# Kernel tuning notes

Hardware: AMD Instinct MI355X
Metric: run time of the kernel (lower is better)

Reference implementation:

```python
import jax, jax.numpy as jnp
import numpy as np

N_NODES = 262144
N_GRAPHS = 1024
FEAT = 256


def setup_inputs() -> dict:
    key = jax.random.key(0)
    ks = jax.random.split(key, 12)
    F = FEAT
    inp = {
        "node_feats": jax.random.normal(ks[0], (N_NODES, F), jnp.float32),
        "g_feats": jax.random.normal(ks[1], (N_GRAPHS, F), jnp.float32),
        "segment_ids": jnp.sort(jax.random.randint(ks[2], (N_NODES,), 0, N_GRAPHS, jnp.int32)),
        "num_graphs": N_GRAPHS,
        # compute_logits: Linear(2F, 1)
        "logit_w": jax.random.normal(ks[3], (1, 2 * F), jnp.float32) / np.sqrt(2 * F),
        "logit_b": jnp.zeros((1,), jnp.float32),
        # project_nodes: Linear(F, F) (dropout is identity at eval)
        "proj_w": jax.random.normal(ks[4], (F, F), jnp.float32) / np.sqrt(F),
        "proj_b": jnp.zeros((F,), jnp.float32),
        # GRUCell(F, F): weight_ih [3F, F], weight_hh [3F, F]
        "w_ih": jax.random.normal(ks[5], (3 * F, F), jnp.float32) / np.sqrt(F),
        "w_hh": jax.random.normal(ks[6], (3 * F, F), jnp.float32) / np.sqrt(F),
        "b_ih": jnp.zeros((3 * F,), jnp.float32),
        "b_hh": jnp.zeros((3 * F,), jnp.float32),
    }
    return inp


def _gru_cell(x, h, w_ih, w_hh, b_ih, b_hh):
    gi = x @ w_ih.T + b_ih          # [B, 3F]
    gh = h @ w_hh.T + b_hh          # [B, 3F]
    i_r, i_z, i_n = jnp.split(gi, 3, axis=-1)
    h_r, h_z, h_n = jnp.split(gh, 3, axis=-1)
    r = jax.nn.sigmoid(i_r + h_r)
    z = jax.nn.sigmoid(i_z + h_z)
    n = jnp.tanh(i_n + r * h_n)
    return (1.0 - z) * n + z * h


def reference(node_feats, g_feats, segment_ids, num_graphs,
              logit_w, logit_b, proj_w, proj_b, w_ih, w_hh, b_ih, b_hh):
    # broadcast_nodes(g, relu(g_feats)) -> gather per-graph feats to nodes
    bcast = jax.nn.relu(g_feats)[segment_ids]                    # [N, F]
    cat = jnp.concatenate([bcast, node_feats], axis=-1)          # [N, 2F]
    z = jax.nn.leaky_relu(cat @ logit_w.T + logit_b, 0.01)       # [N, 1]
    # segment softmax over nodes of each graph (dgl.softmax_nodes)
    zf = z[:, 0]
    m = jax.ops.segment_max(zf, segment_ids, num_segments=num_graphs)
    e = jnp.exp(zf - m[segment_ids])
    s = jax.ops.segment_sum(e, segment_ids, num_segments=num_graphs)
    a = (e / s[segment_ids])[:, None]                            # [N, 1]
    # project_nodes (dropout = identity at eval)
    hv = node_feats @ proj_w.T + proj_b                          # [N, F]
    # attention-weighted segment sum (dgl.sum_nodes with weight 'a')
    g_repr = jax.ops.segment_sum(a * hv, segment_ids, num_segments=num_graphs)  # [B, F]
    return _gru_cell(jax.nn.elu(g_repr), g_feats, w_ih, w_hh, b_ih, b_hh)
```

## Files before the change

### kernel.cpp

```cpp
#include <hip/hip_runtime.h>
#include <hip/hip_bf16.h>
#include <cstdint>

#define N_NODES  262144
#define N_GRAPHS 1024
#define FEAT     256

using short8 = __attribute__((ext_vector_type(8))) short;
using f32x4  = __attribute__((ext_vector_type(4))) float;

#define MFMA_BF16 __builtin_amdgcn_mfma_f32_16x16x32_bf16

__device__ __forceinline__ unsigned short f2bf(float f){
    unsigned u = __float_as_uint(f);
    u = u + 0x7FFFu + ((u >> 16) & 1u);
    return (unsigned short)(u >> 16);
}
__device__ __forceinline__ float sigmoidf_(float x){ return 1.0f/(1.0f+__expf(-x)); }

__global__ __launch_bounds__(256) void glogit_kernel(
        const float* __restrict__ gf, const float* __restrict__ lw,
        const float* __restrict__ lb, float* __restrict__ glog){
    int wid  = (blockIdx.x*blockDim.x + threadIdx.x) >> 6;
    int lane = threadIdx.x & 63;
    if (wid >= N_GRAPHS) return;
    float4 g = ((const float4*)gf)[wid*64 + lane];
    float4 w = ((const float4*)lw)[lane];
    float p = fmaxf(g.x,0.f)*w.x + fmaxf(g.y,0.f)*w.y +
              fmaxf(g.z,0.f)*w.z + fmaxf(g.w,0.f)*w.w;
    #pragma unroll
    for (int m=1;m<64;m<<=1) p += __shfl_xor(p, m, 64);
    if (lane==0) glog[wid] = p + lb[0];
}

__global__ __launch_bounds__(256) void convert_kernel(
        const float* __restrict__ gf,  const float* __restrict__ pw,
        const float* __restrict__ wih, const float* __restrict__ whh,
        unsigned short* __restrict__ h_bf,  unsigned short* __restrict__ pw_bf,
        unsigned short* __restrict__ wih_bf, unsigned short* __restrict__ whh_bf){
    int i = blockIdx.x*blockDim.x + threadIdx.x;
    const float* src; unsigned short* dst; int base;
    if      (i <  65536){ src=gf;  dst=h_bf;   base=i;        }
    else if (i <  81920){ src=pw;  dst=pw_bf;  base=i-65536;  }
    else if (i < 131072){ src=wih; dst=wih_bf; base=i-81920;  }
    else                { src=whh; dst=whh_bf; base=i-131072; }
    float4 v = ((const float4*)src)[base];
    ushort4 o; o.x=f2bf(v.x); o.y=f2bf(v.y); o.z=f2bf(v.z); o.w=f2bf(v.w);
    ((ushort4*)dst)[base] = o;
}

__global__ __launch_bounds__(256) void pass1_kernel(
        const float* __restrict__ nf, const int* __restrict__ seg,
        const float* __restrict__ glog, const float* __restrict__ lw1,
        float* __restrict__ num, float* __restrict__ den){
    const int NPW = 32;
    int wid  = (blockIdx.x*blockDim.x + threadIdx.x) >> 6;
    int lane = threadIdx.x & 63;
    int n0   = wid * NPW;
    float4 w4 = ((const float4*)lw1)[lane];
    const float4* nf4 = (const float4*)nf;

    float a0=0.f,a1=0.f,a2=0.f,a3=0.f,dacc=0.f;
    int   cur = seg[n0];
    float gl  = glog[cur];
    float4 x  = nf4[(size_t)n0*64 + lane];
    int    s  = cur;

    for (int i=0;i<NPW;i++){
        float4 xc = x; int sc = s;
        if (i+1 < NPW){
            x = nf4[(size_t)(n0+i+1)*64 + lane];
            s = seg[n0+i+1];
        }
        if (sc != cur){
            atomicAdd(&num[cur*FEAT + lane*4+0], a0);
            atomicAdd(&num[cur*FEAT + lane*4+1], a1);
            atomicAdd(&num[cur*FEAT + lane*4+2], a2);
            atomicAdd(&num[cur*FEAT + lane*4+3], a3);
            if (lane==0) atomicAdd(&den[cur], dacc);
            a0=a1=a2=a3=0.f; dacc=0.f; cur=sc; gl=glog[sc];
        }
        float p = xc.x*w4.x + xc.y*w4.y + xc.z*w4.z + xc.w*w4.w;
        #pragma unroll
        for (int m=1;m<64;m<<=1) p += __shfl_xor(p, m, 64);
        float q  = gl + p;
        float zf = q > 0.f ? q : 0.01f*q;
        float e  = __expf(zf);
        a0 += e*xc.x; a1 += e*xc.y; a2 += e*xc.z; a3 += e*xc.w;
        if (lane==0) dacc += e;
    }
    atomicAdd(&num[cur*FEAT + lane*4+0], a0);
    atomicAdd(&num[cur*FEAT + lane*4+1], a1);
    atomicAdd(&num[cur*FEAT + lane*4+2], a2);
    atomicAdd(&num[cur*FEAT + lane*4+3], a3);
    if (lane==0) atomicAdd(&den[cur], dacc);
}

__global__ __launch_bounds__(256) void gemm1_kernel(
        const float* __restrict__ num, const float* __restrict__ den,
        const unsigned short* __restrict__ pw_bf, const float* __restrict__ pb,
        unsigned short* __restrict__ x_bf){
    int wid  = (blockIdx.x*blockDim.x + threadIdx.x) >> 6;
    int lane = threadIdx.x & 63;
    int rtile = (wid >> 4) * 16;
    int ctile = (wid & 15) * 16;
    int arow = rtile + (lane & 15);
    int brow = ctile + (lane & 15);
    int kgrp = (lane >> 4) * 8;
    float dv  = den[arow];
    float inv = dv > 0.f ? 1.0f/dv : 0.f;
    f32x4 acc = {0.f,0.f,0.f,0.f};
    #pragma unroll
    for (int kk=0; kk<FEAT; kk+=32){
        int kb = kk + kgrp;
        float4 u0 = *(const float4*)(num + arow*FEAT + kb);
        float4 u1 = *(const float4*)(num + arow*FEAT + kb + 4);
        short8 af;
        af[0]=(short)f2bf(u0.x*inv); af[1]=(short)f2bf(u0.y*inv);
        af[2]=(short)f2bf(u0.z*inv); af[3]=(short)f2bf(u0.w*inv);
        af[4]=(short)f2bf(u1.x*inv); af[5]=(short)f2bf(u1.y*inv);
        af[6]=(short)f2bf(u1.z*inv); af[7]=(short)f2bf(u1.w*inv);
        short8 bfr = *(const short8*)(pw_bf + brow*FEAT + kb);
        acc = MFMA_BF16(af, bfr, acc, 0, 0, 0);
    }
    #pragma unroll
    for (int r=0;r<4;r++){
        int row = rtile + (lane>>4)*4 + r;
        int col = ctile + (lane & 15);
        float g  = acc[r] + pb[col];
        float xv = g > 0.f ? g : (__expf(g) - 1.0f);
        x_bf[row*FEAT + col] = f2bf(xv);
    }
}

__global__ __launch_bounds__(256) void gemm2_kernel(
        const unsigned short* __restrict__ x_bf, const unsigned short* __restrict__ h_bf,
        const unsigned short* __restrict__ wih_bf, const unsigned short* __restrict__ whh_bf,
        const float* __restrict__ bih, const float* __restrict__ bhh,
        const float* __restrict__ gf, float* __restrict__ out){
    int wid  = (blockIdx.x*blockDim.x + threadIdx.x) >> 6;
    int lane = threadIdx.x & 63;
    int rtile = (wid >> 4) * 16;
    int ctile = (wid & 15) * 16;
    int arow = rtile + (lane & 15);
    int wrow = ctile + (lane & 15);
    int kgrp = (lane >> 4) * 8;
    f32x4 ir={0,0,0,0}, iz={0,0,0,0}, inn={0,0,0,0};
    f32x4 hr={0,0,0,0}, hz={0,0,0,0}, hnn={0,0,0,0};
    #pragma unroll
    for (int kk=0; kk<FEAT; kk+=32){
        int kb = kk + kgrp;
        short8 ax  = *(const short8*)(x_bf  + arow*FEAT + kb);
        short8 ah  = *(const short8*)(h_bf  + arow*FEAT + kb);
        short8 bir = *(const short8*)(wih_bf + (wrow      )*FEAT + kb);
        short8 biz = *(const short8*)(wih_bf + (wrow + 256)*FEAT + kb);
        short8 bin = *(const short8*)(wih_bf + (wrow + 512)*FEAT + kb);
        short8 bhr = *(const short8*)(whh_bf + (wrow      )*FEAT + kb);
        short8 bhz = *(const short8*)(whh_bf + (wrow + 256)*FEAT + kb);
        short8 bhn = *(const short8*)(whh_bf + (wrow + 512)*FEAT + kb);
        ir  = MFMA_BF16(ax, bir, ir , 0,0,0);
        iz  = MFMA_BF16(ax, biz, iz , 0,0,0);
        inn = MFMA_BF16(ax, bin, inn, 0,0,0);
        hr  = MFMA_BF16(ah, bhr, hr , 0,0,0);
        hz  = MFMA_BF16(ah, bhz, hz , 0,0,0);
        hnn = MFMA_BF16(ah, bhn, hnn, 0,0,0);
    }
    #pragma unroll
    for (int r=0;r<4;r++){
        int row = rtile + (lane>>4)*4 + r;
        int col = ctile + (lane & 15);
        float vir = ir [r] + bih[col      ];
        float viz = iz [r] + bih[col + 256];
        float vin = inn[r] + bih[col + 512];
        float vhr = hr [r] + bhh[col      ];
        float vhz = hz [r] + bhh[col + 256];
        float vhn = hnn[r] + bhh[col + 512];
        float rg = sigmoidf_(vir + vhr);
        float zg = sigmoidf_(viz + vhz);
        float ng = tanhf(vin + rg*vhn);
        float h  = gf[row*FEAT + col];
        out[row*FEAT + col] = (1.f - zg)*ng + zg*h;
    }
}

extern "C" void kernel_launch(void* const* d_in, const int* in_sizes, int n_in,
                              void* d_out, int out_size, void* d_ws, size_t ws_size,
                              hipStream_t stream){
    const float* nf  = (const float*)d_in[0];
    const float* gf  = (const float*)d_in[1];
    const int*   seg = (const int*)  d_in[2];
    const float* lw  = (const float*)d_in[4];
    const float* lb  = (const float*)d_in[5];
    const float* pw  = (const float*)d_in[6];
    const float* pb  = (const float*)d_in[7];
    const float* wih = (const float*)d_in[8];
    const float* whh = (const float*)d_in[9];
    const float* bih = (const float*)d_in[10];
    const float* bhh = (const float*)d_in[11];
    float* out = (float*)d_out;

    float* num  = (float*)d_ws;
    float* den  = num + N_GRAPHS*FEAT;
    float* glog = den + N_GRAPHS;
    unsigned short* h_bf   = (unsigned short*)(glog + N_GRAPHS);
    unsigned short* pw_bf  = h_bf   + N_GRAPHS*FEAT;
    unsigned short* wih_bf = pw_bf  + FEAT*FEAT;
    unsigned short* whh_bf = wih_bf + 3*FEAT*FEAT;
    unsigned short* x_bf   = whh_bf + 3*FEAT*FEAT;

    hipMemsetAsync(d_ws, 0, (size_t)(N_GRAPHS*FEAT + N_GRAPHS)*sizeof(float), stream);
    glogit_kernel <<<N_GRAPHS/4, 256, 0, stream>>>(gf, lw, lb, glog);
    convert_kernel<<<704,        256, 0, stream>>>(gf, pw, wih, whh, h_bf, pw_bf, wih_bf, whh_bf);
    pass1_kernel  <<<2048,       256, 0, stream>>>(nf, seg, glog, lw + FEAT, num, den);
    gemm1_kernel  <<<256,        256, 0, stream>>>(num, den, pw_bf, pb, x_bf);
    gemm2_kernel  <<<256,        256, 0, stream>>>(x_bf, h_bf, wih_bf, whh_bf, bih, bhh, gf, out);
}
```

Baseline: 410.1 us.

## Merge prep kernels, fuse both GEMMs via LDS, use nontemporal node loads

The memset, the graph-logit kernel and the weight-conversion kernel become one prep launch that zeroes the accumulators with regular stores. The projection GEMM plus ELU and the GRU GEMM are fused into one kernel: each block computes a 16-row slab of the projected features into shared memory and then runs the GRU gates on it, so the x_bf round trip through global memory goes away. The node-feature stream in pass1 uses nontemporal loads to reduce cache pollution. The trade-off is fewer launches and less traffic against only 64 blocks for the fused GEMM, which lowers parallelism in that stage.

```diff
diff --git a/kernel.cpp b/kernel.cpp
--- a/kernel.cpp
+++ b/kernel.cpp
@@ -18,35 +18,39 @@
 }
 __device__ __forceinline__ float sigmoidf_(float x){ return 1.0f/(1.0f+__expf(-x)); }
 
-__global__ __launch_bounds__(256) void glogit_kernel(
-        const float* __restrict__ gf, const float* __restrict__ lw,
-        const float* __restrict__ lb, float* __restrict__ glog){
-    int wid  = (blockIdx.x*blockDim.x + threadIdx.x) >> 6;
-    int lane = threadIdx.x & 63;
-    if (wid >= N_GRAPHS) return;
-    float4 g = ((const float4*)gf)[wid*64 + lane];
-    float4 w = ((const float4*)lw)[lane];
-    float p = fmaxf(g.x,0.f)*w.x + fmaxf(g.y,0.f)*w.y +
-              fmaxf(g.z,0.f)*w.z + fmaxf(g.w,0.f)*w.w;
-    #pragma unroll
-    for (int m=1;m<64;m<<=1) p += __shfl_xor(p, m, 64);
-    if (lane==0) glog[wid] = p + lb[0];
-}
-
-__global__ __launch_bounds__(256) void convert_kernel(
+__global__ __launch_bounds__(256) void prep_kernel(
         const float* __restrict__ gf,  const float* __restrict__ pw,
         const float* __restrict__ wih, const float* __restrict__ whh,
+        const float* __restrict__ lw,  const float* __restrict__ lb,
         unsigned short* __restrict__ h_bf,  unsigned short* __restrict__ pw_bf,
-        unsigned short* __restrict__ wih_bf, unsigned short* __restrict__ whh_bf){
-    int i = blockIdx.x*blockDim.x + threadIdx.x;
-    const float* src; unsigned short* dst; int base;
-    if      (i <  65536){ src=gf;  dst=h_bf;   base=i;        }
-    else if (i <  81920){ src=pw;  dst=pw_bf;  base=i-65536;  }
-    else if (i < 131072){ src=wih; dst=wih_bf; base=i-81920;  }
-    else                { src=whh; dst=whh_bf; base=i-131072; }
-    float4 v = ((const float4*)src)[base];
-    ushort4 o; o.x=f2bf(v.x); o.y=f2bf(v.y); o.z=f2bf(v.z); o.w=f2bf(v.w);
-    ((ushort4*)dst)[base] = o;
+        unsigned short* __restrict__ wih_bf, unsigned short* __restrict__ whh_bf,
+        float* __restrict__ num, float* __restrict__ glog){
+    int b = blockIdx.x;
+    if (b < 704){
+        int i = b*256 + threadIdx.x;
+        const float* src; unsigned short* dst; int base;
+        if      (i <  65536){ src=gf;  dst=h_bf;   base=i;        }
+        else if (i <  81920){ src=pw;  dst=pw_bf;  base=i-65536;  }
+        else if (i < 131072){ src=wih; dst=wih_bf; base=i-81920;  }
+        else                { src=whh; dst=whh_bf; base=i-131072; }
+        float4 v = ((const float4*)src)[base];
+        ushort4 o; o.x=f2bf(v.x); o.y=f2bf(v.y); o.z=f2bf(v.z); o.w=f2bf(v.w);
+        ((ushort4*)dst)[base] = o;
+    } else if (b < 961){
+        int i = (b-704)*256 + threadIdx.x;
+        float4 z = {0.f,0.f,0.f,0.f};
+        ((float4*)num)[i] = z;
+    } else {
+        int wid  = (b-961)*4 + (threadIdx.x >> 6);
+        int lane = threadIdx.x & 63;
+        float4 g = ((const float4*)gf)[wid*64 + lane];
+        float4 w = ((const float4*)lw)[lane];
+        float p = fmaxf(g.x,0.f)*w.x + fmaxf(g.y,0.f)*w.y +
+                  fmaxf(g.z,0.f)*w.z + fmaxf(g.w,0.f)*w.w;
+        #pragma unroll
+        for (int m=1;m<64;m<<=1) p += __shfl_xor(p, m, 64);
+        if (lane==0) glog[wid] = p + lb[0];
+    }
 }
 
 __global__ __launch_bounds__(256) void pass1_kernel(
@@ -57,19 +61,19 @@
     int wid  = (blockIdx.x*blockDim.x + threadIdx.x) >> 6;
     int lane = threadIdx.x & 63;
     int n0   = wid * NPW;
-    float4 w4 = ((const float4*)lw1)[lane];
-    const float4* nf4 = (const float4*)nf;
+    f32x4 w4 = ((const f32x4*)lw1)[lane];
+    const f32x4* nf4 = (const f32x4*)nf;
 
     float a0=0.f,a1=0.f,a2=0.f,a3=0.f,dacc=0.f;
     int   cur = seg[n0];
     float gl  = glog[cur];
-    float4 x  = nf4[(size_t)n0*64 + lane];
+    f32x4 x   = __builtin_nontemporal_load(nf4 + (size_t)n0*64 + lane);
     int    s  = cur;
 
     for (int i=0;i<NPW;i++){
-        float4 xc = x; int sc = s;
+        f32x4 xc = x; int sc = s;
         if (i+1 < NPW){
-            x = nf4[(size_t)(n0+i+1)*64 + lane];
+            x = __builtin_nontemporal_load(nf4 + (size_t)(n0+i+1)*64 + lane);
             s = seg[n0+i+1];
         }
         if (sc != cur){
@@ -80,13 +84,13 @@
             if (lane==0) atomicAdd(&den[cur], dacc);
             a0=a1=a2=a3=0.f; dacc=0.f; cur=sc; gl=glog[sc];
         }
-        float p = xc.x*w4.x + xc.y*w4.y + xc.z*w4.z + xc.w*w4.w;
+        float p = xc[0]*w4[0] + xc[1]*w4[1] + xc[2]*w4[2] + xc[3]*w4[3];
         #pragma unroll
         for (int m=1;m<64;m<<=1) p += __shfl_xor(p, m, 64);
         float q  = gl + p;
         float zf = q > 0.f ? q : 0.01f*q;
         float e  = __expf(zf);
-        a0 += e*xc.x; a1 += e*xc.y; a2 += e*xc.z; a3 += e*xc.w;
+        a0 += e*xc[0]; a1 += e*xc[1]; a2 += e*xc[2]; a3 += e*xc[3];
         if (lane==0) dacc += e;
     }
     atomicAdd(&num[cur*FEAT + lane*4+0], a0);
@@ -96,90 +100,100 @@
     if (lane==0) atomicAdd(&den[cur], dacc);
 }
 
-__global__ __launch_bounds__(256) void gemm1_kernel(
+__global__ __launch_bounds__(256) void gemm_fused_kernel(
         const float* __restrict__ num, const float* __restrict__ den,
         const unsigned short* __restrict__ pw_bf, const float* __restrict__ pb,
-        unsigned short* __restrict__ x_bf){
-    int wid  = (blockIdx.x*blockDim.x + threadIdx.x) >> 6;
-    int lane = threadIdx.x & 63;
-    int rtile = (wid >> 4) * 16;
-    int ctile = (wid & 15) * 16;
-    int arow = rtile + (lane & 15);
-    int brow = ctile + (lane & 15);
-    int kgrp = (lane >> 4) * 8;
-    float dv  = den[arow];
-    float inv = dv > 0.f ? 1.0f/dv : 0.f;
-    f32x4 acc = {0.f,0.f,0.f,0.f};
-    #pragma unroll
-    for (int kk=0; kk<FEAT; kk+=32){
-        int kb = kk + kgrp;
-        float4 u0 = *(const float4*)(num + arow*FEAT + kb);
-        float4 u1 = *(const float4*)(num + arow*FEAT + kb + 4);
-        short8 af;
-        af[0]=(short)f2bf(u0.x*inv); af[1]=(short)f2bf(u0.y*inv);
-        af[2]=(short)f2bf(u0.z*inv); af[3]=(short)f2bf(u0.w*inv);
-        af[4]=(short)f2bf(u1.x*inv); af[5]=(short)f2bf(u1.y*inv);
-        af[6]=(short)f2bf(u1.z*inv); af[7]=(short)f2bf(u1.w*inv);
-        short8 bfr = *(const short8*)(pw_bf + brow*FEAT + kb);
-        acc = MFMA_BF16(af, bfr, acc, 0, 0, 0);
-    }
-    #pragma unroll
-    for (int r=0;r<4;r++){
-        int row = rtile + (lane>>4)*4 + r;
-        int col = ctile + (lane & 15);
-        float g  = acc[r] + pb[col];
-        float xv = g > 0.f ? g : (__expf(g) - 1.0f);
-        x_bf[row*FEAT + col] = f2bf(xv);
-    }
-}
-
-__global__ __launch_bounds__(256) void gemm2_kernel(
-        const unsigned short* __restrict__ x_bf, const unsigned short* __restrict__ h_bf,
+        const unsigned short* __restrict__ h_bf,
         const unsigned short* __restrict__ wih_bf, const unsigned short* __restrict__ whh_bf,
         const float* __restrict__ bih, const float* __restrict__ bhh,
         const float* __restrict__ gf, float* __restrict__ out){
-    int wid  = (blockIdx.x*blockDim.x + threadIdx.x) >> 6;
+    __shared__ unsigned short x_s[16][264];
+    int r0   = blockIdx.x * 16;
+    int wave = threadIdx.x >> 6;
     int lane = threadIdx.x & 63;
-    int rtile = (wid >> 4) * 16;
-    int ctile = (wid & 15) * 16;
-    int arow = rtile + (lane & 15);
-    int wrow = ctile + (lane & 15);
+    int rq   = lane & 15;
     int kgrp = (lane >> 4) * 8;
-    f32x4 ir={0,0,0,0}, iz={0,0,0,0}, inn={0,0,0,0};
-    f32x4 hr={0,0,0,0}, hz={0,0,0,0}, hnn={0,0,0,0};
-    #pragma unroll
-    for (int kk=0; kk<FEAT; kk+=32){
-        int kb = kk + kgrp;
-        short8 ax  = *(const short8*)(x_bf  + arow*FEAT + kb);
-        short8 ah  = *(const short8*)(h_bf  + arow*FEAT + kb);
-        short8 bir = *(const short8*)(wih_bf + (wrow      )*FEAT + kb);
-        short8 biz = *(const short8*)(wih_bf + (wrow + 256)*FEAT + kb);
-        short8 bin = *(const short8*)(wih_bf + (wrow + 512)*FEAT + kb);
-        short8 bhr = *(const short8*)(whh_bf + (wrow      )*FEAT + kb);
-        short8 bhz = *(const short8*)(whh_bf + (wrow + 256)*FEAT + kb);
-        short8 bhn = *(const short8*)(whh_bf + (wrow + 512)*FEAT + kb);
-        ir  = MFMA_BF16(ax, bir, ir , 0,0,0);
-        iz  = MFMA_BF16(ax, biz, iz , 0,0,0);
-        inn = MFMA_BF16(ax, bin, inn, 0,0,0);
-        hr  = MFMA_BF16(ah, bhr, hr , 0,0,0);
-        hz  = MFMA_BF16(ah, bhz, hz , 0,0,0);
-        hnn = MFMA_BF16(ah, bhn, hnn, 0,0,0);
-    }
-    #pragma unroll
-    for (int r=0;r<4;r++){
-        int row = rtile + (lane>>4)*4 + r;
-        int col = ctile + (lane & 15);
-        float vir = ir [r] + bih[col      ];
-        float viz = iz [r] + bih[col + 256];
-        float vin = inn[r] + bih[col + 512];
-        float vhr = hr [r] + bhh[col      ];
-        float vhz = hz [r] + bhh[col + 256];
-        float vhn = hnn[r] + bhh[col + 512];
-        float rg = sigmoidf_(vir + vhr);
-        float zg = sigmoidf_(viz + vhz);
-        float ng = tanhf(vin + rg*vhn);
-        float h  = gf[row*FEAT + col];
-        out[row*FEAT + col] = (1.f - zg)*ng + zg*h;
+    int arow = r0 + rq;
+
+    float dv  = den[arow];
+    float inv = dv > 0.f ? 1.0f/dv : 0.f;
+    short8 af[8];
+    #pragma unroll
+    for (int t=0;t<8;t++){
+        int kb = t*32 + kgrp;
+        float4 u0 = *(const float4*)(num + arow*FEAT + kb);
+        float4 u1 = *(const float4*)(num + arow*FEAT + kb + 4);
+        af[t][0]=(short)f2bf(u0.x*inv); af[t][1]=(short)f2bf(u0.y*inv);
+        af[t][2]=(short)f2bf(u0.z*inv); af[t][3]=(short)f2bf(u0.w*inv);
+        af[t][4]=(short)f2bf(u1.x*inv); af[t][5]=(short)f2bf(u1.y*inv);
+        af[t][6]=(short)f2bf(u1.z*inv); af[t][7]=(short)f2bf(u1.w*inv);
+    }
+    #pragma unroll
+    for (int j=0;j<4;j++){
+        int ct = wave*4 + j;
+        int brow = ct*16 + rq;
+        f32x4 acc = {0.f,0.f,0.f,0.f};
+        #pragma unroll
+        for (int t=0;t<8;t++){
+            short8 bfr = *(const short8*)(pw_bf + brow*FEAT + t*32 + kgrp);
+            acc = MFMA_BF16(af[t], bfr, acc, 0, 0, 0);
+        }
+        #pragma unroll
+        for (int r=0;r<4;r++){
+            int rl  = (lane>>4)*4 + r;
+            int col = ct*16 + rq;
+            float g  = acc[r] + pb[col];
+            float xv = g > 0.f ? g : (__expf(g) - 1.0f);
+            x_s[rl][col] = f2bf(xv);
+        }
+    }
+    __syncthreads();
+
+    short8 ax[8], ah[8];
+    #pragma unroll
+    for (int t=0;t<8;t++){
+        int kb = t*32 + kgrp;
+        ax[t] = *(const short8*)&x_s[rq][kb];
+        ah[t] = *(const short8*)(h_bf + arow*FEAT + kb);
+    }
+    #pragma unroll
+    for (int j=0;j<4;j++){
+        int ct = wave*4 + j;
+        int wrow = ct*16 + rq;
+        f32x4 ir={0,0,0,0}, iz={0,0,0,0}, inn={0,0,0,0};
+        f32x4 hr={0,0,0,0}, hz={0,0,0,0}, hnn={0,0,0,0};
+        #pragma unroll
+        for (int t=0;t<8;t++){
+            int kb = t*32 + kgrp;
+            short8 bir = *(const short8*)(wih_bf + (wrow      )*FEAT + kb);
+            short8 biz = *(const short8*)(wih_bf + (wrow + 256)*FEAT + kb);
+            short8 bin = *(const short8*)(wih_bf + (wrow + 512)*FEAT + kb);
+            short8 bhr = *(const short8*)(whh_bf + (wrow      )*FEAT + kb);
+            short8 bhz = *(const short8*)(whh_bf + (wrow + 256)*FEAT + kb);
+            short8 bhn = *(const short8*)(whh_bf + (wrow + 512)*FEAT + kb);
+            ir  = MFMA_BF16(ax[t], bir, ir , 0,0,0);
+            iz  = MFMA_BF16(ax[t], biz, iz , 0,0,0);
+            inn = MFMA_BF16(ax[t], bin, inn, 0,0,0);
+            hr  = MFMA_BF16(ah[t], bhr, hr , 0,0,0);
+            hz  = MFMA_BF16(ah[t], bhz, hz , 0,0,0);
+            hnn = MFMA_BF16(ah[t], bhn, hnn, 0,0,0);
+        }
+        #pragma unroll
+        for (int r=0;r<4;r++){
+            int row = r0 + (lane>>4)*4 + r;
+            int col = ct*16 + rq;
+            float vir = ir [r] + bih[col      ];
+            float viz = iz [r] + bih[col + 256];
+            float vin = inn[r] + bih[col + 512];
+            float vhr = hr [r] + bhh[col      ];
+            float vhz = hz [r] + bhh[col + 256];
+            float vhn = hnn[r] + bhh[col + 512];
+            float rg = sigmoidf_(vir + vhr);
+            float zg = sigmoidf_(viz + vhz);
+            float ng = tanhf(vin + rg*vhn);
+            float h  = gf[row*FEAT + col];
+            out[row*FEAT + col] = (1.f - zg)*ng + zg*h;
+        }
     }
 }
 
@@ -206,12 +220,10 @@
     unsigned short* pw_bf  = h_bf   + N_GRAPHS*FEAT;
     unsigned short* wih_bf = pw_bf  + FEAT*FEAT;
     unsigned short* whh_bf = wih_bf + 3*FEAT*FEAT;
-    unsigned short* x_bf   = whh_bf + 3*FEAT*FEAT;
-
-    hipMemsetAsync(d_ws, 0, (size_t)(N_GRAPHS*FEAT + N_GRAPHS)*sizeof(float), stream);
-    glogit_kernel <<<N_GRAPHS/4, 256, 0, stream>>>(gf, lw, lb, glog);
-    convert_kernel<<<704,        256, 0, stream>>>(gf, pw, wih, whh, h_bf, pw_bf, wih_bf, whh_bf);
-    pass1_kernel  <<<2048,       256, 0, stream>>>(nf, seg, glog, lw + FEAT, num, den);
-    gemm1_kernel  <<<256,        256, 0, stream>>>(num, den, pw_bf, pb, x_bf);
-    gemm2_kernel  <<<256,        256, 0, stream>>>(x_bf, h_bf, wih_bf, whh_bf, bih, bhh, gf, out);
-}
+
+    prep_kernel      <<<1217, 256, 0, stream>>>(gf, pw, wih, whh, lw, lb,
+                                                h_bf, pw_bf, wih_bf, whh_bf, num, glog);
+    pass1_kernel     <<<2048, 256, 0, stream>>>(nf, seg, glog, lw + FEAT, num, den);
+    gemm_fused_kernel<<<64,   256, 0, stream>>>(num, den, pw_bf, pb, h_bf,
+                                                wih_bf, whh_bf, bih, bhh, gf, out);
+}
```

Result: no change. 412.8 us (+0.7%).
